# Performance work log

Measured on AMD Instinct MI355X. Metric: run time of the kernel, lower is better.

## Reference

```python
import jax, jax.numpy as jnp
import numpy as np

B, C, H, W = 4, 64, 64, 64
CQK = C // 8


def setup_inputs() -> dict:
    key = jax.random.key(0)
    ks = jax.random.split(key, 4)
    x = jax.random.normal(ks[0], (B, C, H, W), dtype=jnp.float32)
    Wq = jax.random.normal(ks[1], (CQK, C), dtype=jnp.float32) * (1.0 / np.sqrt(C))
    bq = jnp.zeros((CQK,), dtype=jnp.float32)
    Wk = jax.random.normal(ks[2], (CQK, C), dtype=jnp.float32) * (1.0 / np.sqrt(C))
    bk = jnp.zeros((CQK,), dtype=jnp.float32)
    Wv = jax.random.normal(ks[3], (C, C), dtype=jnp.float32) * (1.0 / np.sqrt(C))
    bv = jnp.zeros((C,), dtype=jnp.float32)
    gamma = jnp.ones((1,), dtype=jnp.float32)
    return {"x": x, "Wq": Wq, "bq": bq, "Wk": Wk, "bk": bk,
            "Wv": Wv, "bv": bv, "gamma": gamma}


def reference(x, Wq, bq, Wk, bk, Wv, bv, gamma):
    b, c, h, w = x.shape
    n = h * w
    xf = x.reshape(b, c, n)                      # [B, C, N]
    # 1x1 convs == per-pixel linear over channels
    q = jnp.einsum('oc,bcn->bon', Wq, xf) + bq[:, None]   # [B, C/8, N]
    k = jnp.einsum('oc,bcn->bon', Wk, xf) + bk[:, None]   # [B, C/8, N]
    v = jnp.einsum('oc,bcn->bon', Wv, xf) + bv[:, None]   # [B, C, N]
    # attention_map[b,i,j] = <q[:, i], k[:, j]>; softmax over j
    attn = jax.nn.softmax(jnp.einsum('bci,bcj->bij', q, k), axis=-1)  # [B, N, N]
    # out[b,c,i] = sum_j v[b,c,j] * attn[b,i,j]  (bmm(V, attn^T))
    out = jnp.einsum('bcj,bij->bci', v, attn).reshape(b, c, h, w)
    return gamma * out + x
```

## Files before the change

### kernel.cpp

```cpp
#include <hip/hip_runtime.h>
#include <hip/hip_bf16.h>
#include <math.h>

#define NPIX 4096

typedef __attribute__((ext_vector_type(8))) short s8;
typedef __attribute__((ext_vector_type(4))) short s4;
typedef __attribute__((ext_vector_type(16))) float f16v;

static __device__ __forceinline__ unsigned packbf2(float a, float b) {
    union { __hip_bfloat162 h; unsigned u; } x;
    x.h = __float22bfloat162_rn(make_float2(a, b));
    return x.u;
}
static __device__ __forceinline__ float fexp2(float x) {
#if __has_builtin(__builtin_amdgcn_exp2f)
    return __builtin_amdgcn_exp2f(x);
#else
    return exp2f(x);
#endif
}

__global__ __launch_bounds__(256) void prep_kernel(
    const float* __restrict__ x,
    const float* __restrict__ Wq, const float* __restrict__ bq,
    const float* __restrict__ Wk, const float* __restrict__ bk,
    __hip_bfloat16* __restrict__ qbf, __hip_bfloat16* __restrict__ kbf,
    __hip_bfloat16* __restrict__ xbf)
{
    __shared__ float Xp[64][65];
    int t = threadIdx.x;
    int lane = t & 63;
    int grp  = t >> 6;
    int b  = blockIdx.x >> 6;
    int n0 = (blockIdx.x & 63) << 6;

    const float* xb = x + ((size_t)b << 18);
    __hip_bfloat16* xbb = xbf + ((size_t)b << 18);
#pragma unroll
    for (int u = 0; u < 16; ++u) {
        int c = grp + u * 4;
        float v = xb[((size_t)c << 12) + n0 + lane];
        Xp[c][lane] = v;
        xbb[((size_t)c << 12) + n0 + lane] = __float2bfloat16(v);
    }
    __syncthreads();

    int o0 = grp * 2, o1 = o0 + 1;
    float qa0 = bq[o0], qa1 = bq[o1], ka0 = bk[o0], ka1 = bk[o1];
    const float* wq0 = Wq + o0 * 64; const float* wq1 = Wq + o1 * 64;
    const float* wk0 = Wk + o0 * 64; const float* wk1 = Wk + o1 * 64;
#pragma unroll
    for (int c = 0; c < 64; ++c) {
        float xv = Xp[c][lane];
        qa0 = fmaf(wq0[c], xv, qa0);
        qa1 = fmaf(wq1[c], xv, qa1);
        ka0 = fmaf(wk0[c], xv, ka0);
        ka1 = fmaf(wk1[c], xv, ka1);
    }
    qa0 *= 1.4426950408889634f;
    qa1 *= 1.4426950408889634f;
    int pix = b * NPIX + n0 + lane;
    *(__hip_bfloat162*)(qbf + (size_t)pix * 8 + o0) =
        __float22bfloat162_rn(make_float2(qa0, qa1));
    *(__hip_bfloat162*)(kbf + (size_t)pix * 8 + o0) =
        __float22bfloat162_rn(make_float2(ka0, ka1));
}

__global__ __launch_bounds__(512, 4) void flash_fused_kernel(
    const __hip_bfloat16* __restrict__ qbf, const __hip_bfloat16* __restrict__ kbf,
    const __hip_bfloat16* __restrict__ xbf,
    const float* __restrict__ Wv, const float* __restrict__ bv,
    const float* __restrict__ x, const float* __restrict__ gamma,
    float* __restrict__ out)
{
    __shared__ __align__(16) char pool[35200];
    unsigned short* Xs = (unsigned short*)pool;

    int t = threadIdx.x;
    int w    = t >> 6;
    int lane = t & 63;
    int l32  = lane & 31;
    int lh   = lane >> 5;

    int b  = blockIdx.x >> 7;
    int i0 = (blockIdx.x & 127) << 5;

    const s8 zero8 = {0, 0, 0, 0, 0, 0, 0, 0};

    s8 qf;
    {
        s8 qv = *(const s8*)(qbf + ((size_t)(b * NPIX + i0 + l32) << 3));
        qf = (lh == 0) ? qv : zero8;
    }

    f16v acc[2];
    f16v zero16;
#pragma unroll
    for (int r = 0; r < 16; ++r) { acc[0][r] = 0.f; acc[1][r] = 0.f; zero16[r] = 0.f; }
    float lsum = 0.f;

    const __hip_bfloat16* kb = kbf + ((size_t)(b * NPIX) << 3);
    const unsigned short* xg = (const unsigned short*)xbf + ((size_t)b << 18);

    int c = (w << 3) + (t & 7), seg = (t >> 3) & 7;
    const unsigned short* xsrc = xg + ((size_t)c << 12) + seg * 32;
    int xdst = c * 260 + seg * 32;

    uint2 pv[8];
    s8 kf;
    {
        const unsigned short* p = xsrc;
#pragma unroll
        for (int u = 0; u < 8; ++u) pv[u] = *(const uint2*)(p + u * 4);
        kf = *(const s8*)(kb + ((size_t)(w * 32 + l32) << 3));
    }

    for (int jt = 0; jt < 16; ++jt) {
        __syncthreads();

        {
            unsigned short* dstp = Xs + xdst;
#pragma unroll
            for (int u = 0; u < 8; ++u) *(uint2*)(dstp + u * 4) = pv[u];
        }

        f16v sC = __builtin_amdgcn_mfma_f32_32x32x16_bf16(kf, qf, zero16, 0, 0, 0);
        float e[16];
#pragma unroll
        for (int r = 0; r < 16; ++r) e[r] = fexp2(sC[r]);
#pragma unroll
        for (int r = 0; r < 16; ++r) lsum += e[r];
        unsigned P2[8];
#pragma unroll
        for (int s = 0; s < 8; ++s) P2[s] = packbf2(e[2 * s], e[2 * s + 1]);

        __syncthreads();

        {
            int jn = ((jt + 1) & 15) << 8;
            const unsigned short* p = xsrc + jn;
#pragma unroll
            for (int u = 0; u < 8; ++u) pv[u] = *(const uint2*)(p + u * 4);
            kf = *(const s8*)(kb + ((size_t)(jn + w * 32 + l32) << 3));
        }

#if __has_builtin(__builtin_amdgcn_mfma_f32_32x32x8bf16_1k)
#pragma unroll
        for (int cm = 0; cm < 2; ++cm) {
            const unsigned short* xrow = Xs + (cm * 32 + l32) * 260 + w * 32 + lh * 4;
#pragma unroll
            for (int q = 0; q < 4; ++q) {
                s4 xf = *(const s4*)(xrow + q * 8);
                union { uint2 u; s4 v; } pu;
                pu.u.x = P2[2 * q]; pu.u.y = P2[2 * q + 1];
                acc[cm] = __builtin_amdgcn_mfma_f32_32x32x8bf16_1k(xf, pu.v, acc[cm], 0, 0, 0);
            }
        }
#else
        {
            unsigned X0 = __shfl_xor(P2[0], 32), X1 = __shfl_xor(P2[1], 32);
            unsigned X2 = __shfl_xor(P2[2], 32), X3 = __shfl_xor(P2[3], 32);
            unsigned X4 = __shfl_xor(P2[4], 32), X5 = __shfl_xor(P2[5], 32);
            unsigned X6 = __shfl_xor(P2[6], 32), X7 = __shfl_xor(P2[7], 32);
            union { uint4 u[2]; s8 v[2]; } bf;
            bf.u[0].x = lh ? X2 : P2[0]; bf.u[0].y = lh ? X3 : P2[1];
            bf.u[0].z = lh ? P2[2] : X0; bf.u[0].w = lh ? P2[3] : X1;
            bf.u[1].x = lh ? X6 : P2[4]; bf.u[1].y = lh ? X7 : P2[5];
            bf.u[1].z = lh ? P2[6] : X4; bf.u[1].w = lh ? P2[7] : X5;
#pragma unroll
            for (int cm = 0; cm < 2; ++cm) {
                const unsigned short* xrow = Xs + (cm * 32 + l32) * 260 + w * 32 + lh * 8;
#pragma unroll
                for (int q = 0; q < 2; ++q) {
                    union { uint2 u[2]; s8 v; } xu;
                    xu.u[0] = *(const uint2*)(xrow + q * 16);
                    xu.u[1] = *(const uint2*)(xrow + q * 16 + 4);
                    acc[cm] = __builtin_amdgcn_mfma_f32_32x32x16_bf16(xu.v, bf.v[q], acc[cm], 0, 0, 0);
                }
            }
        }
#endif
    }

    float* OshA = (float*)pool;
    float* OshB = (float*)(pool + 8704);
    float* Linv = (float*)(pool + 17408);
    float* bvs  = (float*)(pool + 17536);
    float* Wvs  = (float*)(pool + 17792);
    float* Lsh  = (float*)(pool + 34176);

    lsum += __shfl_xor(lsum, 32);
    if (lh == 0) Lsh[w * 32 + l32] = lsum;

    float* Og = (w >> 2) ? OshB : OshA;
    for (int s = 0; s < 4; ++s) {
        __syncthreads();
        if ((w & 3) == s) {
#pragma unroll
            for (int cm = 0; cm < 2; ++cm)
#pragma unroll
                for (int r = 0; r < 16; ++r) {
                    int cc = cm * 32 + (r & 3) + 8 * (r >> 2) + 4 * lh;
                    float* p = Og + l32 * 68 + cc;
                    if (s == 0) *p = acc[cm][r];
                    else        *p += acc[cm][r];
                }
        }
    }
    __syncthreads();

    if (t < 32) {
        float lt = 0.f;
#pragma unroll
        for (int ww = 0; ww < 8; ++ww) lt += Lsh[ww * 32 + t];
        Linv[t] = 1.0f / lt;
    }
    if (t < 64) bvs[t] = bv[t];
    {
        const float4* wsrc = (const float4*)Wv;
        float4* wdst = (float4*)Wvs;
        wdst[t] = wsrc[t];
        wdst[t + 512] = wsrc[t + 512];
    }
    __syncthreads();

    {
        int i  = t & 31;
        int cg = t >> 5;
        float inv = Linv[i];
        float res[4] = {0.f, 0.f, 0.f, 0.f};
#pragma unroll 4
        for (int cb = 0; cb < 16; ++cb) {
            float4 oa = *(const float4*)(OshA + i * 68 + cb * 4);
            float4 ob = *(const float4*)(OshB + i * 68 + cb * 4);
            float4 o = make_float4(oa.x + ob.x, oa.y + ob.y, oa.z + ob.z, oa.w + ob.w);
#pragma unroll
            for (int k = 0; k < 4; ++k) {
                const float4 wv4 = *(const float4*)(Wvs + (cg * 4 + k) * 64 + cb * 4);
                res[k] = fmaf(wv4.x, o.x, fmaf(wv4.y, o.y, fmaf(wv4.z, o.z, fmaf(wv4.w, o.w, res[k]))));
            }
        }
        float g = gamma[0];
        const float* xr = x + ((size_t)b << 18) + i0;
        float* outp = out + ((size_t)b << 18) + i0;
#pragma unroll
        for (int k = 0; k < 4; ++k) {
            int cch = cg * 4 + k;
            float attn = fmaf(res[k], inv, bvs[cch]);
            size_t off = ((size_t)cch << 12) + i;
            outp[off] = fmaf(g, attn, xr[off]);
        }
    }
}

extern "C" void kernel_launch(void* const* d_in, const int* in_sizes, int n_in,
                              void* d_out, int out_size, void* d_ws, size_t ws_size,
                              hipStream_t stream) {
    const float* x     = (const float*)d_in[0];
    const float* Wq    = (const float*)d_in[1];
    const float* bq    = (const float*)d_in[2];
    const float* Wk    = (const float*)d_in[3];
    const float* bk    = (const float*)d_in[4];
    const float* Wv    = (const float*)d_in[5];
    const float* bv    = (const float*)d_in[6];
    const float* gamma = (const float*)d_in[7];
    float* out = (float*)d_out;

    __hip_bfloat16* qbf = (__hip_bfloat16*)d_ws;
    __hip_bfloat16* kbf = qbf + (size_t)4 * NPIX * 8;
    __hip_bfloat16* xbf = kbf + (size_t)4 * NPIX * 8;

    prep_kernel<<<256, 256, 0, stream>>>(x, Wq, bq, Wk, bk, qbf, kbf, xbf);
    flash_fused_kernel<<<512, 512, 0, stream>>>(qbf, kbf, xbf, Wv, bv, x, gamma, out);
}
```

Measured before the change: 112.6 us.

## Split attention key range across two blocks and add combine kernel

The flash kernel now splits the 4096 key pixels into two halves handled by separate blocks, doubling the grid to 1024 blocks. Each block writes unnormalized partial outputs and row sums to workspace, and a new combine kernel sums the halves and applies the Wv projection, bias and residual. This works because no running max is used, so partials add directly. The prep kernel is also reorganized to split Q and K computation across two blocks with 512 threads and packed 16-byte stores. The aim is more parallelism and occupancy, at the cost of an extra launch and an 8 MB partial-output round trip through memory.

Result: slower. 121.9 us (+8.2%).

```diff
diff --git a/kernel.cpp b/kernel.cpp
--- a/kernel.cpp
+++ b/kernel.cpp
@@ -21,7 +21,7 @@
 #endif
 }
 
-__global__ __launch_bounds__(256) void prep_kernel(
+__global__ __launch_bounds__(512) void prep_kernel(
     const float* __restrict__ x,
     const float* __restrict__ Wq, const float* __restrict__ bq,
     const float* __restrict__ Wk, const float* __restrict__ bk,
@@ -29,50 +29,50 @@
     __hip_bfloat16* __restrict__ xbf)
 {
     __shared__ float Xp[64][65];
+    __shared__ unsigned short Qs[64][8];
     int t = threadIdx.x;
-    int lane = t & 63;
-    int grp  = t >> 6;
-    int b  = blockIdx.x >> 6;
-    int n0 = (blockIdx.x & 63) << 6;
+    int p = t & 63;
+    int g = t >> 6;
+    int bid = blockIdx.x;
+    int og = bid & 1;
+    int n0 = ((bid >> 1) & 63) << 6;
+    int b  = bid >> 7;
 
     const float* xb = x + ((size_t)b << 18);
     __hip_bfloat16* xbb = xbf + ((size_t)b << 18);
 #pragma unroll
-    for (int u = 0; u < 16; ++u) {
-        int c = grp + u * 4;
-        float v = xb[((size_t)c << 12) + n0 + lane];
-        Xp[c][lane] = v;
-        xbb[((size_t)c << 12) + n0 + lane] = __float2bfloat16(v);
+    for (int u = 0; u < 8; ++u) {
+        int c = g + (u << 3);
+        float v = xb[((size_t)c << 12) + n0 + p];
+        Xp[c][p] = v;
+        if ((og == 0) ? (u < 4) : (u >= 4))
+            xbb[((size_t)c << 12) + n0 + p] = __float2bfloat16(v);
     }
     __syncthreads();
 
-    int o0 = grp * 2, o1 = o0 + 1;
-    float qa0 = bq[o0], qa1 = bq[o1], ka0 = bk[o0], ka1 = bk[o1];
-    const float* wq0 = Wq + o0 * 64; const float* wq1 = Wq + o1 * 64;
-    const float* wk0 = Wk + o0 * 64; const float* wk1 = Wk + o1 * 64;
-#pragma unroll
-    for (int c = 0; c < 64; ++c) {
-        float xv = Xp[c][lane];
-        qa0 = fmaf(wq0[c], xv, qa0);
-        qa1 = fmaf(wq1[c], xv, qa1);
-        ka0 = fmaf(wk0[c], xv, ka0);
-        ka1 = fmaf(wk1[c], xv, ka1);
-    }
-    qa0 *= 1.4426950408889634f;
-    qa1 *= 1.4426950408889634f;
-    int pix = b * NPIX + n0 + lane;
-    *(__hip_bfloat162*)(qbf + (size_t)pix * 8 + o0) =
-        __float22bfloat162_rn(make_float2(qa0, qa1));
-    *(__hip_bfloat162*)(kbf + (size_t)pix * 8 + o0) =
-        __float22bfloat162_rn(make_float2(ka0, ka1));
+    const float* W  = og ? Wk : Wq;
+    const float* bb = og ? bk : bq;
+    const float* wr = W + g * 64;
+    float acc = bb[g];
+#pragma unroll
+    for (int c = 0; c < 64; ++c) acc = fmaf(wr[c], Xp[c][p], acc);
+    if (!og) acc *= 1.4426950408889634f;
+
+    union { __hip_bfloat16 h; unsigned short u; } cv;
+    cv.h = __float2bfloat16(acc);
+    Qs[p][g] = cv.u;
+    __syncthreads();
+
+    if (t < 64) {
+        __hip_bfloat16* dst = (og ? kbf : qbf) + ((size_t)(b * NPIX + n0 + t) << 3);
+        *(s8*)dst = *(const s8*)&Qs[t][0];
+    }
 }
 
 __global__ __launch_bounds__(512, 4) void flash_fused_kernel(
     const __hip_bfloat16* __restrict__ qbf, const __hip_bfloat16* __restrict__ kbf,
     const __hip_bfloat16* __restrict__ xbf,
-    const float* __restrict__ Wv, const float* __restrict__ bv,
-    const float* __restrict__ x, const float* __restrict__ gamma,
-    float* __restrict__ out)
+    float* __restrict__ opart, float* __restrict__ lpart)
 {
     __shared__ __align__(16) char pool[35200];
     unsigned short* Xs = (unsigned short*)pool;
@@ -83,8 +83,11 @@
     int l32  = lane & 31;
     int lh   = lane >> 5;
 
-    int b  = blockIdx.x >> 7;
-    int i0 = (blockIdx.x & 127) << 5;
+    int bid = blockIdx.x;
+    int jh  = bid & 1;
+    int i0  = ((bid >> 1) & 127) << 5;
+    int b   = bid >> 8;
+    int jbase = jh << 3;
 
     const s8 zero8 = {0, 0, 0, 0, 0, 0, 0, 0};
 
@@ -110,13 +113,13 @@
     uint2 pv[8];
     s8 kf;
     {
-        const unsigned short* p = xsrc;
+        const unsigned short* p = xsrc + (jbase << 8);
 #pragma unroll
         for (int u = 0; u < 8; ++u) pv[u] = *(const uint2*)(p + u * 4);
-        kf = *(const s8*)(kb + ((size_t)(w * 32 + l32) << 3));
-    }
-
-    for (int jt = 0; jt < 16; ++jt) {
+        kf = *(const s8*)(kb + ((size_t)((jbase << 8) + w * 32 + l32) << 3));
+    }
+
+    for (int lt = 0; lt < 8; ++lt) {
         __syncthreads();
 
         {
@@ -138,7 +141,7 @@
         __syncthreads();
 
         {
-            int jn = ((jt + 1) & 15) << 8;
+            int jn = (jbase + ((lt + 1) & 7)) << 8;
             const unsigned short* p = xsrc + jn;
 #pragma unroll
             for (int u = 0; u < 8; ++u) pv[u] = *(const uint2*)(p + u * 4);
@@ -185,9 +188,6 @@
 
     float* OshA = (float*)pool;
     float* OshB = (float*)(pool + 8704);
-    float* Linv = (float*)(pool + 17408);
-    float* bvs  = (float*)(pool + 17536);
-    float* Wvs  = (float*)(pool + 17792);
     float* Lsh  = (float*)(pool + 34176);
 
     lsum += __shfl_xor(lsum, 32);
@@ -211,11 +211,47 @@
     __syncthreads();
 
     if (t < 32) {
-        float lt = 0.f;
-#pragma unroll
-        for (int ww = 0; ww < 8; ++ww) lt += Lsh[ww * 32 + t];
-        Linv[t] = 1.0f / lt;
-    }
+        float lt2 = 0.f;
+#pragma unroll
+        for (int ww = 0; ww < 8; ++ww) lt2 += Lsh[ww * 32 + t];
+        lpart[(size_t)bid * 32 + t] = lt2;
+    }
+    {
+        float* Op = opart + (size_t)bid * 2048;
+        int i = t >> 4, sg = t & 15;
+        float4 oa = *(const float4*)(OshA + i * 68 + sg * 4);
+        float4 ob = *(const float4*)(OshB + i * 68 + sg * 4);
+        *(float4*)(Op + i * 64 + sg * 4) =
+            make_float4(oa.x + ob.x, oa.y + ob.y, oa.z + ob.z, oa.w + ob.w);
+    }
+}
+
+__global__ __launch_bounds__(512) void combine_kernel(
+    const float* __restrict__ opart, const float* __restrict__ lpart,
+    const float* __restrict__ Wv, const float* __restrict__ bv,
+    const float* __restrict__ x, const float* __restrict__ gamma,
+    float* __restrict__ out)
+{
+    __shared__ float Osum[32 * 68];
+    __shared__ float Linv[32];
+    __shared__ float bvs[64];
+    __shared__ float Wvs[64 * 64];
+
+    int t = threadIdx.x;
+    int cid = blockIdx.x;
+    int b = cid >> 7, it = cid & 127, i0 = it << 5;
+    int base = (b << 8) | (it << 1);
+    const float* p0 = opart + (size_t)base * 2048;
+    const float* p1 = p0 + 2048;
+
+    {
+        int i = t >> 4, sg = t & 15;
+        float4 a  = *(const float4*)(p0 + i * 64 + sg * 4);
+        float4 c4 = *(const float4*)(p1 + i * 64 + sg * 4);
+        *(float4*)(Osum + i * 68 + sg * 4) =
+            make_float4(a.x + c4.x, a.y + c4.y, a.z + c4.z, a.w + c4.w);
+    }
+    if (t < 32) Linv[t] = 1.0f / (lpart[(size_t)base * 32 + t] + lpart[(size_t)base * 32 + 32 + t]);
     if (t < 64) bvs[t] = bv[t];
     {
         const float4* wsrc = (const float4*)Wv;
@@ -225,32 +261,28 @@
     }
     __syncthreads();
 
-    {
-        int i  = t & 31;
-        int cg = t >> 5;
-        float inv = Linv[i];
-        float res[4] = {0.f, 0.f, 0.f, 0.f};
+    int i  = t & 31;
+    int cg = t >> 5;
+    float inv = Linv[i];
+    float res[4] = {0.f, 0.f, 0.f, 0.f};
 #pragma unroll 4
-        for (int cb = 0; cb < 16; ++cb) {
-            float4 oa = *(const float4*)(OshA + i * 68 + cb * 4);
-            float4 ob = *(const float4*)(OshB + i * 68 + cb * 4);
-            float4 o = make_float4(oa.x + ob.x, oa.y + ob.y, oa.z + ob.z, oa.w + ob.w);
-#pragma unroll
-            for (int k = 0; k < 4; ++k) {
-                const float4 wv4 = *(const float4*)(Wvs + (cg * 4 + k) * 64 + cb * 4);
-                res[k] = fmaf(wv4.x, o.x, fmaf(wv4.y, o.y, fmaf(wv4.z, o.z, fmaf(wv4.w, o.w, res[k]))));
-            }
-        }
-        float g = gamma[0];
-        const float* xr = x + ((size_t)b << 18) + i0;
-        float* outp = out + ((size_t)b << 18) + i0;
+    for (int cb = 0; cb < 16; ++cb) {
+        float4 o = *(const float4*)(Osum + i * 68 + cb * 4);
 #pragma unroll
         for (int k = 0; k < 4; ++k) {
-            int cch = cg * 4 + k;
-            float attn = fmaf(res[k], inv, bvs[cch]);
-            size_t off = ((size_t)cch << 12) + i;
-            outp[off] = fmaf(g, attn, xr[off]);
-        }
+            const float4 wv4 = *(const float4*)(Wvs + (cg * 4 + k) * 64 + cb * 4);
+            res[k] = fmaf(wv4.x, o.x, fmaf(wv4.y, o.y, fmaf(wv4.z, o.z, fmaf(wv4.w, o.w, res[k]))));
+        }
+    }
+    float g = gamma[0];
+    const float* xr = x + ((size_t)b << 18) + i0;
+    float* outp = out + ((size_t)b << 18) + i0;
+#pragma unroll
+    for (int k = 0; k < 4; ++k) {
+        int cch = cg * 4 + k;
+        float attn = fmaf(res[k], inv, bvs[cch]);
+        size_t off = ((size_t)cch << 12) + i;
+        outp[off] = fmaf(g, attn, xr[off]);
     }
 }
 
@@ -270,7 +302,10 @@
     __hip_bfloat16* qbf = (__hip_bfloat16*)d_ws;
     __hip_bfloat16* kbf = qbf + (size_t)4 * NPIX * 8;
     __hip_bfloat16* xbf = kbf + (size_t)4 * NPIX * 8;
-
-    prep_kernel<<<256, 256, 0, stream>>>(x, Wq, bq, Wk, bk, qbf, kbf, xbf);
-    flash_fused_kernel<<<512, 512, 0, stream>>>(qbf, kbf, xbf, Wv, bv, x, gamma, out);
-}
+    float* opart = (float*)(xbf + (size_t)4 * NPIX * 64);
+    float* lpart = opart + (size_t)1024 * 2048;
+
+    prep_kernel<<<512, 512, 0, stream>>>(x, Wq, bq, Wk, bk, qbf, kbf, xbf);
+    flash_fused_kernel<<<1024, 512, 0, stream>>>(qbf, kbf, xbf, opart, lpart);
+    combine_kernel<<<512, 512, 0, stream>>>(opart, lpart, Wv, bv, x, gamma, out);
+}
```

## Use 16-deep bf16 MFMA with permlane32 swap; split prep into Q/K blocks

Applied to the files above, without the earlier changes.

The PV matmul in the flash kernel now always uses the K=16 bf16 MFMA, replacing the older 32x32x8 path that may have been selected before. The operand lanes are rearranged with permlane32_swap, falling back to shuffles when that builtin is unavailable. The prep kernel now runs twice as many 512-thread blocks, each computing either Q or K with one output channel per thread. Results are staged in shared memory so each pixel gets one 16-byte vector store. This aims to halve MFMA issue count and raise prep parallelism, at the cost of each x tile being loaded twice in prep.

Result: no change. 113.8 us (+1.0%).

```diff
diff --git a/kernel.cpp b/kernel.cpp
--- a/kernel.cpp
+++ b/kernel.cpp
@@ -5,7 +5,6 @@
 #define NPIX 4096
 
 typedef __attribute__((ext_vector_type(8))) short s8;
-typedef __attribute__((ext_vector_type(4))) short s4;
 typedef __attribute__((ext_vector_type(16))) float f16v;
 
 static __device__ __forceinline__ unsigned packbf2(float a, float b) {
@@ -21,7 +20,20 @@
 #endif
 }
 
-__global__ __launch_bounds__(256) void prep_kernel(
+static __device__ __forceinline__ void lane_swap(unsigned a, unsigned b, int lh,
+                                                 unsigned &x, unsigned &y) {
+#if __has_builtin(__builtin_amdgcn_permlane32_swap)
+    auto r = __builtin_amdgcn_permlane32_swap((int)a, (int)b, false, false);
+    x = (unsigned)r[0];
+    y = (unsigned)r[1];
+#else
+    unsigned sa = __shfl_xor(a, 32), sb = __shfl_xor(b, 32);
+    x = lh ? sb : a;
+    y = lh ? b : sa;
+#endif
+}
+
+__global__ __launch_bounds__(512) void prep_kernel(
     const float* __restrict__ x,
     const float* __restrict__ Wq, const float* __restrict__ bq,
     const float* __restrict__ Wk, const float* __restrict__ bk,
@@ -29,42 +41,44 @@
     __hip_bfloat16* __restrict__ xbf)
 {
     __shared__ float Xp[64][65];
+    __shared__ unsigned short Qs[64][8];
     int t = threadIdx.x;
-    int lane = t & 63;
-    int grp  = t >> 6;
-    int b  = blockIdx.x >> 6;
-    int n0 = (blockIdx.x & 63) << 6;
+    int p = t & 63;
+    int g = t >> 6;
+    int bid = blockIdx.x;
+    int og = bid & 1;
+    int n0 = ((bid >> 1) & 63) << 6;
+    int b  = bid >> 7;
 
     const float* xb = x + ((size_t)b << 18);
     __hip_bfloat16* xbb = xbf + ((size_t)b << 18);
 #pragma unroll
-    for (int u = 0; u < 16; ++u) {
-        int c = grp + u * 4;
-        float v = xb[((size_t)c << 12) + n0 + lane];
-        Xp[c][lane] = v;
-        xbb[((size_t)c << 12) + n0 + lane] = __float2bfloat16(v);
-    }
-    __syncthreads();
-
-    int o0 = grp * 2, o1 = o0 + 1;
-    float qa0 = bq[o0], qa1 = bq[o1], ka0 = bk[o0], ka1 = bk[o1];
-    const float* wq0 = Wq + o0 * 64; const float* wq1 = Wq + o1 * 64;
-    const float* wk0 = Wk + o0 * 64; const float* wk1 = Wk + o1 * 64;
-#pragma unroll
-    for (int c = 0; c < 64; ++c) {
-        float xv = Xp[c][lane];
-        qa0 = fmaf(wq0[c], xv, qa0);
-        qa1 = fmaf(wq1[c], xv, qa1);
-        ka0 = fmaf(wk0[c], xv, ka0);
-        ka1 = fmaf(wk1[c], xv, ka1);
-    }
-    qa0 *= 1.4426950408889634f;
-    qa1 *= 1.4426950408889634f;
-    int pix = b * NPIX + n0 + lane;
-    *(__hip_bfloat162*)(qbf + (size_t)pix * 8 + o0) =
-        __float22bfloat162_rn(make_float2(qa0, qa1));
-    *(__hip_bfloat162*)(kbf + (size_t)pix * 8 + o0) =
-        __float22bfloat162_rn(make_float2(ka0, ka1));
+    for (int u = 0; u < 8; ++u) {
+        int c = g + (u << 3);
+        float v = xb[((size_t)c << 12) + n0 + p];
+        Xp[c][p] = v;
+        if ((og == 0) ? (u < 4) : (u >= 4))
+            xbb[((size_t)c << 12) + n0 + p] = __float2bfloat16(v);
+    }
+    __syncthreads();
+
+    const float* W  = og ? Wk : Wq;
+    const float* bb = og ? bk : bq;
+    const float* wr = W + g * 64;
+    float acc = bb[g];
+#pragma unroll
+    for (int c = 0; c < 64; ++c) acc = fmaf(wr[c], Xp[c][p], acc);
+    if (!og) acc *= 1.4426950408889634f;
+
+    union { __hip_bfloat16 h; unsigned short u; } cv;
+    cv.h = __float2bfloat16(acc);
+    Qs[p][g] = cv.u;
+    __syncthreads();
+
+    if (t < 64) {
+        __hip_bfloat16* dst = (og ? kbf : qbf) + ((size_t)(b * NPIX + n0 + t) << 3);
+        *(s8*)dst = *(const s8*)&Qs[t][0];
+    }
 }
 
 __global__ __launch_bounds__(512, 4) void flash_fused_kernel(
@@ -145,42 +159,26 @@
             kf = *(const s8*)(kb + ((size_t)(jn + w * 32 + l32) << 3));
         }
 
-#if __has_builtin(__builtin_amdgcn_mfma_f32_32x32x8bf16_1k)
+        unsigned b00, b01, b02, b03, b10, b11, b12, b13;
+        lane_swap(P2[0], P2[2], lh, b00, b02);
+        lane_swap(P2[1], P2[3], lh, b01, b03);
+        lane_swap(P2[4], P2[6], lh, b10, b12);
+        lane_swap(P2[5], P2[7], lh, b11, b13);
+        union { unsigned u[4]; s8 v; } bf0, bf1;
+        bf0.u[0] = b00; bf0.u[1] = b01; bf0.u[2] = b02; bf0.u[3] = b03;
+        bf1.u[0] = b10; bf1.u[1] = b11; bf1.u[2] = b12; bf1.u[3] = b13;
+
 #pragma unroll
         for (int cm = 0; cm < 2; ++cm) {
-            const unsigned short* xrow = Xs + (cm * 32 + l32) * 260 + w * 32 + lh * 4;
-#pragma unroll
-            for (int q = 0; q < 4; ++q) {
-                s4 xf = *(const s4*)(xrow + q * 8);
-                union { uint2 u; s4 v; } pu;
-                pu.u.x = P2[2 * q]; pu.u.y = P2[2 * q + 1];
-                acc[cm] = __builtin_amdgcn_mfma_f32_32x32x8bf16_1k(xf, pu.v, acc[cm], 0, 0, 0);
-            }
-        }
-#else
-        {
-            unsigned X0 = __shfl_xor(P2[0], 32), X1 = __shfl_xor(P2[1], 32);
-            unsigned X2 = __shfl_xor(P2[2], 32), X3 = __shfl_xor(P2[3], 32);
-            unsigned X4 = __shfl_xor(P2[4], 32), X5 = __shfl_xor(P2[5], 32);
-            unsigned X6 = __shfl_xor(P2[6], 32), X7 = __shfl_xor(P2[7], 32);
-            union { uint4 u[2]; s8 v[2]; } bf;
-            bf.u[0].x = lh ? X2 : P2[0]; bf.u[0].y = lh ? X3 : P2[1];
-            bf.u[0].z = lh ? P2[2] : X0; bf.u[0].w = lh ? P2[3] : X1;
-            bf.u[1].x = lh ? X6 : P2[4]; bf.u[1].y = lh ? X7 : P2[5];
-            bf.u[1].z = lh ? P2[6] : X4; bf.u[1].w = lh ? P2[7] : X5;
-#pragma unroll
-            for (int cm = 0; cm < 2; ++cm) {
-                const unsigned short* xrow = Xs + (cm * 32 + l32) * 260 + w * 32 + lh * 8;
-#pragma unroll
-                for (int q = 0; q < 2; ++q) {
-                    union { uint2 u[2]; s8 v; } xu;
-                    xu.u[0] = *(const uint2*)(xrow + q * 16);
-                    xu.u[1] = *(const uint2*)(xrow + q * 16 + 4);
-                    acc[cm] = __builtin_amdgcn_mfma_f32_32x32x16_bf16(xu.v, bf.v[q], acc[cm], 0, 0, 0);
-                }
-            }
-        }
-#endif
+            const unsigned short* xrow = Xs + (cm * 32 + l32) * 260 + w * 32 + lh * 8;
+            union { uint2 u2[2]; s8 v; } xu0, xu1;
+            xu0.u2[0] = *(const uint2*)(xrow);
+            xu0.u2[1] = *(const uint2*)(xrow + 4);
+            acc[cm] = __builtin_amdgcn_mfma_f32_32x32x16_bf16(xu0.v, bf0.v, acc[cm], 0, 0, 0);
+            xu1.u2[0] = *(const uint2*)(xrow + 16);
+            xu1.u2[1] = *(const uint2*)(xrow + 20);
+            acc[cm] = __builtin_amdgcn_mfma_f32_32x32x16_bf16(xu1.v, bf1.v, acc[cm], 0, 0, 0);
+        }
     }
 
     float* OshA = (float*)pool;
@@ -271,6 +269,6 @@
     __hip_bfloat16* kbf = qbf + (size_t)4 * NPIX * 8;
     __hip_bfloat16* xbf = kbf + (size_t)4 * NPIX * 8;
 
-    prep_kernel<<<256, 256, 0, stream>>>(x, Wq, bq, Wk, bk, qbf, kbf, xbf);
+    prep_kernel<<<512, 512, 0, stream>>>(x, Wq, bq, Wk, bk, qbf, kbf, xbf);
     flash_fused_kernel<<<512, 512, 0, stream>>>(qbf, kbf, xbf, Wv, bv, x, gamma, out);
 }
```
